# Kernel tuning notes

Hardware: AMD Instinct MI355X
Metric: run time of the kernel (lower is better)

The kernel has to match this reference:

```python
import jax, jax.numpy as jnp
from jax import lax
import numpy as np

T, B, N_POINTS = 512, 256, 34
N_HIDDEN, N_TARGET = 512, 16


def setup_inputs() -> dict:
    key = jax.random.key(0)
    ks = jax.random.split(key, 7)
    s_ih = 1.0 / np.sqrt(N_HIDDEN)
    return {
        "points": jax.random.normal(ks[0], (T, B, N_POINTS), dtype=jnp.float32),
        "W_ih": jax.random.uniform(ks[1], (4 * N_HIDDEN, N_POINTS), dtype=jnp.float32, minval=-s_ih, maxval=s_ih),
        "W_hh": jax.random.uniform(ks[2], (4 * N_HIDDEN, N_HIDDEN), dtype=jnp.float32, minval=-s_ih, maxval=s_ih),
        "b_ih": jax.random.uniform(ks[3], (4 * N_HIDDEN,), dtype=jnp.float32, minval=-s_ih, maxval=s_ih),
        "b_hh": jax.random.uniform(ks[4], (4 * N_HIDDEN,), dtype=jnp.float32, minval=-s_ih, maxval=s_ih),
        "W_lin": jax.random.uniform(ks[5], (N_TARGET, N_HIDDEN), dtype=jnp.float32, minval=-s_ih, maxval=s_ih),
        "b_lin": jax.random.uniform(ks[6], (N_TARGET,), dtype=jnp.float32, minval=-s_ih, maxval=s_ih),
    }


def reference(points, W_ih, W_hh, b_ih, b_hh, W_lin, b_lin):
    # points: [T, B, n_points]; PyTorch LSTM gate order: i, f, g, o
    H = W_hh.shape[1]
    Bsz = points.shape[1]
    # Precompute input projection for all timesteps: [T, B, 4H]
    x_proj = jnp.einsum('tbi,gi->tbg', points, W_ih) + b_ih + b_hh

    def step(carry, xt):
        h, c = carry
        gates = xt + h @ W_hh.T  # [B, 4H]
        i, f, g, o = jnp.split(gates, 4, axis=-1)
        i = jax.nn.sigmoid(i)
        f = jax.nn.sigmoid(f)
        g = jnp.tanh(g)
        o = jax.nn.sigmoid(o)
        c_new = f * c + i * g
        h_new = o * jnp.tanh(c_new)
        return (h_new, c_new), h_new

    h0 = jnp.zeros((Bsz, H), dtype=points.dtype)
    c0 = jnp.zeros((Bsz, H), dtype=points.dtype)
    _, hs = lax.scan(step, (h0, c0), x_proj)  # hs: [T, B, H]

    logits = hs.reshape(-1, H) @ W_lin.T + b_lin  # [T*B, n_target]
    return jax.nn.softmax(logits, axis=1)
```

## Files before the change

kernel.cpp:

```cpp
#include <hip/hip_runtime.h>

#define TT 512
#define BT 256
#define NP 34
#define HH 512
#define SENT 0xAAAAAAAAu

typedef short bf16x8 __attribute__((ext_vector_type(8)));
typedef float f32x4 __attribute__((ext_vector_type(4)));

static __device__ __forceinline__ unsigned short f2bf(float x) {
  unsigned int u = __float_as_uint(x);
  return (unsigned short)((u + 0x7fffu + ((u >> 16) & 1u)) >> 16);
}

template <int CTRL>
static __device__ __forceinline__ float dppq(float x) {
  return __int_as_float(
      __builtin_amdgcn_mov_dpp(__float_as_int(x), CTRL, 0xF, 0xF, true));
}

static __device__ __forceinline__ float rcpf(float x) {
  return __builtin_amdgcn_rcpf(x);
}

static __device__ __forceinline__ void load8_coh(const unsigned long long* p,
                                                 unsigned long long o[8]) {
  asm volatile(
      "global_load_dwordx2 %0, %8, off sc0 sc1\n\t"
      "global_load_dwordx2 %1, %9, off sc0 sc1\n\t"
      "global_load_dwordx2 %2, %10, off sc0 sc1\n\t"
      "global_load_dwordx2 %3, %11, off sc0 sc1\n\t"
      "global_load_dwordx2 %4, %12, off sc0 sc1\n\t"
      "global_load_dwordx2 %5, %13, off sc0 sc1\n\t"
      "global_load_dwordx2 %6, %14, off sc0 sc1\n\t"
      "global_load_dwordx2 %7, %15, off sc0 sc1\n\t"
      "s_waitcnt vmcnt(0)"
      : "=&v"(o[0]), "=&v"(o[1]), "=&v"(o[2]), "=&v"(o[3]),
        "=&v"(o[4]), "=&v"(o[5]), "=&v"(o[6]), "=&v"(o[7])
      : "v"(p), "v"(p + 256), "v"(p + 512), "v"(p + 768),
        "v"(p + 1024), "v"(p + 1280), "v"(p + 1536), "v"(p + 1792)
      : "memory");
}

__global__ void __launch_bounds__(256, 1) lstm_coop(
    const float* __restrict__ Whh, const float* __restrict__ Wih,
    const float* __restrict__ bih, const float* __restrict__ bhh,
    const unsigned short* __restrict__ Ax,
    unsigned short* hs)
{
  extern __shared__ char smem[];
  unsigned short* Wl = (unsigned short*)smem;
  unsigned short* stg = (unsigned short*)(smem + 131072);

  const int tid = threadIdx.x;
  const int g = blockIdx.x & 15;
  const int n = blockIdx.x >> 4;
  const int bbase = g * 16;

  for (int idx = tid; idx < 128 * 512; idx += 256) {
    int r = idx >> 9, k = idx & 511;
    int grow = (r & 3) * 512 + n * 32 + (r >> 2);
    float v = Whh[(size_t)grow * 512 + k];
    int c = k >> 3;
    Wl[r * 512 + ((c ^ (r & 7)) << 3) + (k & 7)] = f2bf(v);
  }

  const int lane = tid & 63;
  const int w = tid >> 6;
  const int m = lane & 15;
  const int ko = lane >> 4;
  const int r0 = 32 * w + m;
  const int q = m & 3;
  const int jj = m >> 2;
  const int j0 = 8 * w + jj;
  const int j1 = j0 + 4;
  const int mx = m & 7;

  float bi0[4], bi1[4];
#pragma unroll
  for (int gg = 0; gg < 4; ++gg) {
    int gr0 = gg * 512 + n * 32 + j0;
    int gr1 = gg * 512 + n * 32 + j1;
    bi0[gg] = bih[gr0] + bhh[gr0];
    bi1[gg] = bih[gr1] + bhh[gr1];
  }

  bf16x8 bx0a, bx1a, bx0b, bx1b;
  {
    int grow0 = q * 512 + n * 32 + j0;
    int grow1 = q * 512 + n * 32 + j1;
#pragma unroll
    for (int e = 0; e < 8; ++e) {
      int ka = 8 * ko + e;
      int kb = 32 + 8 * ko + e;
      bx0a[e] = (short)f2bf(Wih[grow0 * 34 + ka]);
      bx1a[e] = (short)f2bf(Wih[grow1 * 34 + ka]);
      bx0b[e] = (kb < NP) ? (short)f2bf(Wih[grow0 * 34 + kb]) : (short)0;
      bx1b[e] = (kb < NP) ? (short)f2bf(Wih[grow1 * 34 + kb]) : (short)0;
    }
  }
  __syncthreads();

  const bool q0 = (q == 0), q1 = (q == 1), q2 = (q == 2);
  float cc0 = 0.f, cc1 = 0.f;

  bf16x8 xv0, xv1;
  {
    const unsigned short* xb = Ax + ((size_t)0 * BT + bbase + m) * 64;
    xv0 = *(const bf16x8*)(xb + (ko << 3));
    xv1 = *(const bf16x8*)(xb + 32 + (ko << 3));
  }

  for (int t = 0; t < TT; ++t) {
    unsigned long long hv[8];
    if (t > 0) {
      const unsigned long long* pb =
          (const unsigned long long*)(hs + ((size_t)(t - 1) * BT + bbase) * HH) + tid;
      int guard = 0;
      for (;;) {
        load8_coh(pb, hv);
        unsigned ok = 1u;
#pragma unroll
        for (int u = 0; u < 8; ++u) {
          unsigned long long x = hv[u];
          ok &= ((unsigned)x != SENT) & ((unsigned)(x >> 32) != SENT) ? 1u : 0u;
        }
        if (ok) break;
        if (++guard > (1 << 18)) break;
      }
    } else {
#pragma unroll
      for (int u = 0; u < 8; ++u) hv[u] = 0ull;
    }

    bf16x8 xn0, xn1;
    {
      int tn = (t + 1 < TT) ? t + 1 : t;
      const unsigned short* xb = Ax + ((size_t)tn * BT + bbase + m) * 64;
      xn0 = *(const bf16x8*)(xb + (ko << 3));
      xn1 = *(const bf16x8*)(xb + 32 + (ko << 3));
    }

    unsigned short* st = stg + (t & 1) * 8192;
#pragma unroll
    for (int u = 0; u < 8; ++u) {
      int idx = u * 256 + tid;
      int mm = idx >> 7, cu = idx & 127;
      int c16 = cu >> 1, half = cu & 1;
      *(unsigned long long*)&st[mm * 512 + ((c16 ^ (mm & 7)) << 3) + (half << 2)] = hv[u];
    }
    __syncthreads();

    f32x4 a0a = {0.f, 0.f, 0.f, 0.f}, a0b = {0.f, 0.f, 0.f, 0.f};
    f32x4 a1a = {0.f, 0.f, 0.f, 0.f}, a1b = {0.f, 0.f, 0.f, 0.f};
#pragma unroll
    for (int s = 0; s < 16; ++s) {
      int cs = (((4 * s + ko) ^ mx) << 3);
      bf16x8 av = *(const bf16x8*)&st[m * 512 + cs];
      bf16x8 bv0 = *(const bf16x8*)&Wl[r0 * 512 + cs];
      bf16x8 bv1 = *(const bf16x8*)&Wl[(r0 + 16) * 512 + cs];
      if (s & 1) {
        a0b = __builtin_amdgcn_mfma_f32_16x16x32_bf16(av, bv0, a0b, 0, 0, 0);
        a1b = __builtin_amdgcn_mfma_f32_16x16x32_bf16(av, bv1, a1b, 0, 0, 0);
      } else {
        a0a = __builtin_amdgcn_mfma_f32_16x16x32_bf16(av, bv0, a0a, 0, 0, 0);
        a1a = __builtin_amdgcn_mfma_f32_16x16x32_bf16(av, bv1, a1a, 0, 0, 0);
      }
    }
    a0a = __builtin_amdgcn_mfma_f32_16x16x32_bf16(xv0, bx0a, a0a, 0, 0, 0);
    a1a = __builtin_amdgcn_mfma_f32_16x16x32_bf16(xv0, bx1a, a1a, 0, 0, 0);
    a0b = __builtin_amdgcn_mfma_f32_16x16x32_bf16(xv1, bx0b, a0b, 0, 0, 0);
    a1b = __builtin_amdgcn_mfma_f32_16x16x32_bf16(xv1, bx1b, a1b, 0, 0, 0);
    f32x4 A0 = a0a + a0b;
    f32x4 A1 = a1a + a1b;

    float own0 = q0 ? A0.x : q1 ? A0.y : q2 ? A0.z : A0.w;
    float t1s0 = q0 ? A0.w : q1 ? A0.x : q2 ? A0.y : A0.z;
    float t2s0 = q0 ? A0.z : q1 ? A0.w : q2 ? A0.x : A0.y;
    float t3s0 = q0 ? A0.y : q1 ? A0.z : q2 ? A0.w : A0.x;
    float r1_0 = dppq<0x39>(t1s0);
    float r2_0 = dppq<0x4E>(t2s0);
    float r3_0 = dppq<0x93>(t3s0);
    float own1 = q0 ? A1.x : q1 ? A1.y : q2 ? A1.z : A1.w;
    float t1s1 = q0 ? A1.w : q1 ? A1.x : q2 ? A1.y : A1.z;
    float t2s1 = q0 ? A1.z : q1 ? A1.w : q2 ? A1.x : A1.y;
    float t3s1 = q0 ? A1.y : q1 ? A1.z : q2 ? A1.w : A1.x;
    float r1_1 = dppq<0x39>(t1s1);
    float r2_1 = dppq<0x4E>(t2s1);
    float r3_1 = dppq<0x93>(t3s1);
    float gi0 = (q0 ? own0 : q1 ? r3_0 : q2 ? r2_0 : r1_0) + bi0[0];
    float gf0 = (q0 ? r1_0 : q1 ? own0 : q2 ? r3_0 : r2_0) + bi0[1];
    float gg0 = (q0 ? r2_0 : q1 ? r1_0 : q2 ? own0 : r3_0) + bi0[2];
    float go0 = (q0 ? r3_0 : q1 ? r2_0 : q2 ? r1_0 : own0) + bi0[3];
    float gi1 = (q0 ? own1 : q1 ? r3_1 : q2 ? r2_1 : r1_1) + bi1[0];
    float gf1 = (q0 ? r1_1 : q1 ? own1 : q2 ? r3_1 : r2_1) + bi1[1];
    float gg1 = (q0 ? r2_1 : q1 ? r1_1 : q2 ? own1 : r3_1) + bi1[2];
    float go1 = (q0 ? r3_1 : q1 ? r2_1 : q2 ? r1_1 : own1) + bi1[3];

    float ii0 = rcpf(1.f + __expf(-gi0));
    float ff0 = rcpf(1.f + __expf(-gf0));
    float tg0 = 2.f * rcpf(1.f + __expf(-2.f * gg0)) - 1.f;
    float oo0 = rcpf(1.f + __expf(-go0));
    cc0 = ff0 * cc0 + ii0 * tg0;
    float h0 = oo0 * (2.f * rcpf(1.f + __expf(-2.f * cc0)) - 1.f);

    float ii1 = rcpf(1.f + __expf(-gi1));
    float ff1 = rcpf(1.f + __expf(-gf1));
    float tg1 = 2.f * rcpf(1.f + __expf(-2.f * gg1)) - 1.f;
    float oo1 = rcpf(1.f + __expf(-go1));
    cc1 = ff1 * cc1 + ii1 * tg1;
    float h1 = oo1 * (2.f * rcpf(1.f + __expf(-2.f * cc1)) - 1.f);

    float h0p = __shfl_xor(h0, 4);
    float h1p = __shfl_xor(h1, 4);
    unsigned p0 = (unsigned)f2bf(h0) | ((unsigned)f2bf(h0p) << 16);
    unsigned p1 = (unsigned)f2bf(h1) | ((unsigned)f2bf(h1p) << 16);
    unsigned s0 = (unsigned)__shfl_xor((int)p0, 8);
    unsigned s1 = (unsigned)__shfl_xor((int)p1, 8);
    if (!(jj & 1)) {
      unsigned long long val = (jj == 0)
          ? (((unsigned long long)s0 << 32) | p0)
          : (((unsigned long long)p1 << 32) | s1);
      size_t uidx = ((size_t)t * BT + bbase + 4 * ko + q) * 128 +
                    8 * n + 2 * w + (jj >> 1);
      __hip_atomic_store((unsigned long long*)hs + uidx, val,
                         __ATOMIC_RELAXED, __HIP_MEMORY_SCOPE_AGENT);
    }
    xv0 = xn0;
    xv1 = xn1;
  }
}

__global__ void __launch_bounds__(256) prep_ax(const float* __restrict__ pts,
                                               unsigned short* __restrict__ Ax) {
  size_t i = (size_t)blockIdx.x * 256 + threadIdx.x;
  int k = (int)(i & 63);
  size_t tb = i >> 6;
  float v = (k < NP) ? pts[tb * NP + k] : 0.f;
  Ax[i] = f2bf(v);
}

__global__ void __launch_bounds__(256) head_kernel(const unsigned short* __restrict__ hs,
                                                   const float* __restrict__ Wlin,
                                                   const float* __restrict__ blin,
                                                   float* __restrict__ out) {
  __shared__ float wl[16 * 513];
  __shared__ float bl[16];
  __shared__ unsigned short hl[16 * 520];
  const int tid = threadIdx.x;
  for (int i = tid; i < 16 * 512; i += 256) wl[(i >> 9) * 513 + (i & 511)] = Wlin[i];
  if (tid < 16) bl[tid] = blin[tid];
  const size_t Rb = (size_t)blockIdx.x * 16;
  const uint4* gsrc = (const uint4*)(hs + Rb * 512);
#pragma unroll
  for (int j = 0; j < 4; ++j) {
    int e8 = tid + 256 * j;
    uint4 v = gsrc[e8];
    int r = e8 >> 6, k = (e8 & 63) << 3;
    *(uint4*)&hl[r * 520 + k] = v;
  }
  __syncthreads();
  const int r = tid >> 4, tg = tid & 15;
  float acc = bl[tg];
  const float* wp = &wl[tg * 513];
#pragma unroll 4
  for (int k8 = 0; k8 < 64; ++k8) {
    uint4 hv = *(const uint4*)&hl[r * 520 + (k8 << 3)];
    const float* w8 = wp + (k8 << 3);
    acc += __uint_as_float(hv.x << 16) * w8[0];
    acc += __uint_as_float(hv.x & 0xffff0000u) * w8[1];
    acc += __uint_as_float(hv.y << 16) * w8[2];
    acc += __uint_as_float(hv.y & 0xffff0000u) * w8[3];
    acc += __uint_as_float(hv.z << 16) * w8[4];
    acc += __uint_as_float(hv.z & 0xffff0000u) * w8[5];
    acc += __uint_as_float(hv.w << 16) * w8[6];
    acc += __uint_as_float(hv.w & 0xffff0000u) * w8[7];
  }
  float mx = acc;
#pragma unroll
  for (int d = 8; d; d >>= 1) mx = fmaxf(mx, __shfl_xor(mx, d, 16));
  float e = __expf(acc - mx);
  float sm = e;
#pragma unroll
  for (int d = 8; d; d >>= 1) sm += __shfl_xor(sm, d, 16);
  out[Rb * 16 + tid] = e / sm;
}

extern "C" void kernel_launch(void* const* d_in, const int* in_sizes, int n_in,
                              void* d_out, int out_size, void* d_ws, size_t ws_size,
                              hipStream_t stream) {
  (void)in_sizes; (void)n_in; (void)out_size; (void)ws_size;
  const float* pts  = (const float*)d_in[0];
  const float* Wih  = (const float*)d_in[1];
  const float* Whh  = (const float*)d_in[2];
  const float* bih  = (const float*)d_in[3];
  const float* bhh  = (const float*)d_in[4];
  const float* Wlin = (const float*)d_in[5];
  const float* blin = (const float*)d_in[6];
  float* out = (float*)d_out;
  char* ws = (char*)d_ws;
  unsigned short* hs = (unsigned short*)ws;
  unsigned short* Ax = (unsigned short*)(ws + 134217728);

  hipMemsetAsync(hs, 0xAA, 134217728, stream);
  prep_ax<<<32768, 256, 0, stream>>>(pts, Ax);
  (void)hipFuncSetAttribute((const void*)lstm_coop,
                            hipFuncAttributeMaxDynamicSharedMemorySize, 163840);
  void* args[6];
  args[0] = (void*)&Whh; args[1] = (void*)&Wih; args[2] = (void*)&bih;
  args[3] = (void*)&bhh; args[4] = (void*)&Ax;  args[5] = (void*)&hs;
  hipLaunchCooperativeKernel((void*)lstm_coop, dim3(256), dim3(256), args, 163840, stream);
  head_kernel<<<8192, 256, 0, stream>>>(hs, Wlin, blin, out);
}
```

Baseline: 1.461 ms.

## Split batch into two interleaved groups to overlap polling with compute

Repartitions the persistent LSTM so each block owns 16 hidden columns for two 16-row batch groups instead of 32 columns for one group. The recurrent h loads for one group are issued asynchronously while the other group's MFMA and gate math run, hiding the cross-block flag latency. In exchange each block holds half the recurrent weights in LDS and does two smaller sync/compute phases per step, adding barriers and producing smaller 8-byte stores.

```diff
diff --git a/kernel.cpp b/kernel.cpp
--- a/kernel.cpp
+++ b/kernel.cpp
@@ -22,6 +22,24 @@
 
 static __device__ __forceinline__ float rcpf(float x) {
   return __builtin_amdgcn_rcpf(x);
+}
+
+static __device__ __forceinline__ void issue8(const unsigned long long* p,
+                                              unsigned long long o[8]) {
+  asm volatile(
+      "global_load_dwordx2 %0, %8, off sc0 sc1\n\t"
+      "global_load_dwordx2 %1, %9, off sc0 sc1\n\t"
+      "global_load_dwordx2 %2, %10, off sc0 sc1\n\t"
+      "global_load_dwordx2 %3, %11, off sc0 sc1\n\t"
+      "global_load_dwordx2 %4, %12, off sc0 sc1\n\t"
+      "global_load_dwordx2 %5, %13, off sc0 sc1\n\t"
+      "global_load_dwordx2 %6, %14, off sc0 sc1\n\t"
+      "global_load_dwordx2 %7, %15, off sc0 sc1"
+      : "=&v"(o[0]), "=&v"(o[1]), "=&v"(o[2]), "=&v"(o[3]),
+        "=&v"(o[4]), "=&v"(o[5]), "=&v"(o[6]), "=&v"(o[7])
+      : "v"(p), "v"(p + 256), "v"(p + 512), "v"(p + 768),
+        "v"(p + 1024), "v"(p + 1280), "v"(p + 1536), "v"(p + 1792)
+      : "memory");
 }
 
 static __device__ __forceinline__ void load8_coh(const unsigned long long* p,
@@ -43,6 +61,17 @@
       : "memory");
 }
 
+static __device__ __forceinline__ unsigned validmask8(
+    const unsigned long long o[8]) {
+  unsigned ok = 1u;
+#pragma unroll
+  for (int u = 0; u < 8; ++u) {
+    unsigned long long x = o[u];
+    ok &= (((unsigned)x != SENT) & ((unsigned)(x >> 32) != SENT)) ? 1u : 0u;
+  }
+  return ok;
+}
+
 __global__ void __launch_bounds__(256, 1) lstm_coop(
     const float* __restrict__ Whh, const float* __restrict__ Wih,
     const float* __restrict__ bih, const float* __restrict__ bhh,
@@ -51,16 +80,18 @@
 {
   extern __shared__ char smem[];
   unsigned short* Wl = (unsigned short*)smem;
-  unsigned short* stg = (unsigned short*)(smem + 131072);
+  unsigned short* stgA = (unsigned short*)(smem + 65536);
+  unsigned short* stgB = (unsigned short*)(smem + 98304);
 
   const int tid = threadIdx.x;
-  const int g = blockIdx.x & 15;
-  const int n = blockIdx.x >> 4;
-  const int bbase = g * 16;
-
-  for (int idx = tid; idx < 128 * 512; idx += 256) {
+  const int n2 = blockIdx.x & 31;
+  const int p = blockIdx.x >> 5;
+  const int bbA = p * 32;
+  const int bbB = p * 32 + 16;
+
+  for (int idx = tid; idx < 64 * 512; idx += 256) {
     int r = idx >> 9, k = idx & 511;
-    int grow = (r & 3) * 512 + n * 32 + (r >> 2);
+    int grow = (r & 3) * 512 + n2 * 16 + (r >> 2);
     float v = Whh[(size_t)grow * 512 + k];
     int c = k >> 3;
     Wl[r * 512 + ((c ^ (r & 7)) << 3) + (k & 7)] = f2bf(v);
@@ -70,79 +101,63 @@
   const int w = tid >> 6;
   const int m = lane & 15;
   const int ko = lane >> 4;
-  const int r0 = 32 * w + m;
+  const int r0 = 16 * w + m;
   const int q = m & 3;
   const int jj = m >> 2;
-  const int j0 = 8 * w + jj;
-  const int j1 = j0 + 4;
+  const int col = n2 * 16 + 4 * w + jj;
   const int mx = m & 7;
-
-  float bi0[4], bi1[4];
+  const bool q0 = (q == 0), q1 = (q == 1), q2 = (q == 2);
+
+  float bi[4];
 #pragma unroll
   for (int gg = 0; gg < 4; ++gg) {
-    int gr0 = gg * 512 + n * 32 + j0;
-    int gr1 = gg * 512 + n * 32 + j1;
-    bi0[gg] = bih[gr0] + bhh[gr0];
-    bi1[gg] = bih[gr1] + bhh[gr1];
-  }
-
-  bf16x8 bx0a, bx1a, bx0b, bx1b;
+    int gr = gg * 512 + col;
+    bi[gg] = bih[gr] + bhh[gr];
+  }
+
+  bf16x8 bxa, bxb;
   {
-    int grow0 = q * 512 + n * 32 + j0;
-    int grow1 = q * 512 + n * 32 + j1;
+    int grow = (r0 & 3) * 512 + n2 * 16 + (r0 >> 2);
 #pragma unroll
     for (int e = 0; e < 8; ++e) {
       int ka = 8 * ko + e;
       int kb = 32 + 8 * ko + e;
-      bx0a[e] = (short)f2bf(Wih[grow0 * 34 + ka]);
-      bx1a[e] = (short)f2bf(Wih[grow1 * 34 + ka]);
-      bx0b[e] = (kb < NP) ? (short)f2bf(Wih[grow0 * 34 + kb]) : (short)0;
-      bx1b[e] = (kb < NP) ? (short)f2bf(Wih[grow1 * 34 + kb]) : (short)0;
+      bxa[e] = (short)f2bf(Wih[grow * 34 + ka]);
+      bxb[e] = (kb < NP) ? (short)f2bf(Wih[grow * 34 + kb]) : (short)0;
     }
   }
   __syncthreads();
 
-  const bool q0 = (q == 0), q1 = (q == 1), q2 = (q == 2);
-  float cc0 = 0.f, cc1 = 0.f;
-
-  bf16x8 xv0, xv1;
+  float ccA = 0.f, ccB = 0.f;
+  unsigned long long pollA[8], pollB[8];
+
+  bf16x8 xvA0, xvA1, xvB0, xvB1;
   {
-    const unsigned short* xb = Ax + ((size_t)0 * BT + bbase + m) * 64;
-    xv0 = *(const bf16x8*)(xb + (ko << 3));
-    xv1 = *(const bf16x8*)(xb + 32 + (ko << 3));
+    const unsigned short* xb = Ax + ((size_t)0 * BT + bbA + m) * 64;
+    xvA0 = *(const bf16x8*)(xb + (ko << 3));
+    xvA1 = *(const bf16x8*)(xb + 32 + (ko << 3));
   }
 
   for (int t = 0; t < TT; ++t) {
-    unsigned long long hv[8];
+    unsigned long long* hv = pollA;
     if (t > 0) {
       const unsigned long long* pb =
-          (const unsigned long long*)(hs + ((size_t)(t - 1) * BT + bbase) * HH) + tid;
-      int guard = 0;
-      for (;;) {
-        load8_coh(pb, hv);
-        unsigned ok = 1u;
-#pragma unroll
-        for (int u = 0; u < 8; ++u) {
-          unsigned long long x = hv[u];
-          ok &= ((unsigned)x != SENT) & ((unsigned)(x >> 32) != SENT) ? 1u : 0u;
+          (const unsigned long long*)(hs + ((size_t)(t - 1) * BT + bbA) * HH) + tid;
+      asm volatile("s_waitcnt vmcnt(0)" ::: "memory");
+      __builtin_amdgcn_sched_barrier(0);
+      if (!validmask8(pollA)) {
+        int guard = 0;
+        for (;;) {
+          load8_coh(pb, pollA);
+          if (validmask8(pollA)) break;
+          if (++guard > (1 << 18)) break;
         }
-        if (ok) break;
-        if (++guard > (1 << 18)) break;
       }
     } else {
 #pragma unroll
-      for (int u = 0; u < 8; ++u) hv[u] = 0ull;
-    }
-
-    bf16x8 xn0, xn1;
-    {
-      int tn = (t + 1 < TT) ? t + 1 : t;
-      const unsigned short* xb = Ax + ((size_t)tn * BT + bbase + m) * 64;
-      xn0 = *(const bf16x8*)(xb + (ko << 3));
-      xn1 = *(const bf16x8*)(xb + 32 + (ko << 3));
-    }
-
-    unsigned short* st = stg + (t & 1) * 8192;
+      for (int u = 0; u < 8; ++u) pollA[u] = 0ull;
+    }
+    unsigned short* st = stgA + (t & 1) * 8192;
 #pragma unroll
     for (int u = 0; u < 8; ++u) {
       int idx = u * 256 + tid;
@@ -151,84 +166,135 @@
       *(unsigned long long*)&st[mm * 512 + ((c16 ^ (mm & 7)) << 3) + (half << 2)] = hv[u];
     }
     __syncthreads();
-
-    f32x4 a0a = {0.f, 0.f, 0.f, 0.f}, a0b = {0.f, 0.f, 0.f, 0.f};
-    f32x4 a1a = {0.f, 0.f, 0.f, 0.f}, a1b = {0.f, 0.f, 0.f, 0.f};
-#pragma unroll
-    for (int s = 0; s < 16; ++s) {
-      int cs = (((4 * s + ko) ^ mx) << 3);
-      bf16x8 av = *(const bf16x8*)&st[m * 512 + cs];
-      bf16x8 bv0 = *(const bf16x8*)&Wl[r0 * 512 + cs];
-      bf16x8 bv1 = *(const bf16x8*)&Wl[(r0 + 16) * 512 + cs];
-      if (s & 1) {
-        a0b = __builtin_amdgcn_mfma_f32_16x16x32_bf16(av, bv0, a0b, 0, 0, 0);
-        a1b = __builtin_amdgcn_mfma_f32_16x16x32_bf16(av, bv1, a1b, 0, 0, 0);
-      } else {
-        a0a = __builtin_amdgcn_mfma_f32_16x16x32_bf16(av, bv0, a0a, 0, 0, 0);
-        a1a = __builtin_amdgcn_mfma_f32_16x16x32_bf16(av, bv1, a1a, 0, 0, 0);
-      }
-    }
-    a0a = __builtin_amdgcn_mfma_f32_16x16x32_bf16(xv0, bx0a, a0a, 0, 0, 0);
-    a1a = __builtin_amdgcn_mfma_f32_16x16x32_bf16(xv0, bx1a, a1a, 0, 0, 0);
-    a0b = __builtin_amdgcn_mfma_f32_16x16x32_bf16(xv1, bx0b, a0b, 0, 0, 0);
-    a1b = __builtin_amdgcn_mfma_f32_16x16x32_bf16(xv1, bx1b, a1b, 0, 0, 0);
-    f32x4 A0 = a0a + a0b;
-    f32x4 A1 = a1a + a1b;
-
-    float own0 = q0 ? A0.x : q1 ? A0.y : q2 ? A0.z : A0.w;
-    float t1s0 = q0 ? A0.w : q1 ? A0.x : q2 ? A0.y : A0.z;
-    float t2s0 = q0 ? A0.z : q1 ? A0.w : q2 ? A0.x : A0.y;
-    float t3s0 = q0 ? A0.y : q1 ? A0.z : q2 ? A0.w : A0.x;
-    float r1_0 = dppq<0x39>(t1s0);
-    float r2_0 = dppq<0x4E>(t2s0);
-    float r3_0 = dppq<0x93>(t3s0);
-    float own1 = q0 ? A1.x : q1 ? A1.y : q2 ? A1.z : A1.w;
-    float t1s1 = q0 ? A1.w : q1 ? A1.x : q2 ? A1.y : A1.z;
-    float t2s1 = q0 ? A1.z : q1 ? A1.w : q2 ? A1.x : A1.y;
-    float t3s1 = q0 ? A1.y : q1 ? A1.z : q2 ? A1.w : A1.x;
-    float r1_1 = dppq<0x39>(t1s1);
-    float r2_1 = dppq<0x4E>(t2s1);
-    float r3_1 = dppq<0x93>(t3s1);
-    float gi0 = (q0 ? own0 : q1 ? r3_0 : q2 ? r2_0 : r1_0) + bi0[0];
-    float gf0 = (q0 ? r1_0 : q1 ? own0 : q2 ? r3_0 : r2_0) + bi0[1];
-    float gg0 = (q0 ? r2_0 : q1 ? r1_0 : q2 ? own0 : r3_0) + bi0[2];
-    float go0 = (q0 ? r3_0 : q1 ? r2_0 : q2 ? r1_0 : own0) + bi0[3];
-    float gi1 = (q0 ? own1 : q1 ? r3_1 : q2 ? r2_1 : r1_1) + bi1[0];
-    float gf1 = (q0 ? r1_1 : q1 ? own1 : q2 ? r3_1 : r2_1) + bi1[1];
-    float gg1 = (q0 ? r2_1 : q1 ? r1_1 : q2 ? own1 : r3_1) + bi1[2];
-    float go1 = (q0 ? r3_1 : q1 ? r2_1 : q2 ? r1_1 : own1) + bi1[3];
-
-    float ii0 = rcpf(1.f + __expf(-gi0));
-    float ff0 = rcpf(1.f + __expf(-gf0));
-    float tg0 = 2.f * rcpf(1.f + __expf(-2.f * gg0)) - 1.f;
-    float oo0 = rcpf(1.f + __expf(-go0));
-    cc0 = ff0 * cc0 + ii0 * tg0;
-    float h0 = oo0 * (2.f * rcpf(1.f + __expf(-2.f * cc0)) - 1.f);
-
-    float ii1 = rcpf(1.f + __expf(-gi1));
-    float ff1 = rcpf(1.f + __expf(-gf1));
-    float tg1 = 2.f * rcpf(1.f + __expf(-2.f * gg1)) - 1.f;
-    float oo1 = rcpf(1.f + __expf(-go1));
-    cc1 = ff1 * cc1 + ii1 * tg1;
-    float h1 = oo1 * (2.f * rcpf(1.f + __expf(-2.f * cc1)) - 1.f);
-
-    float h0p = __shfl_xor(h0, 4);
-    float h1p = __shfl_xor(h1, 4);
-    unsigned p0 = (unsigned)f2bf(h0) | ((unsigned)f2bf(h0p) << 16);
-    unsigned p1 = (unsigned)f2bf(h1) | ((unsigned)f2bf(h1p) << 16);
-    unsigned s0 = (unsigned)__shfl_xor((int)p0, 8);
-    unsigned s1 = (unsigned)__shfl_xor((int)p1, 8);
-    if (!(jj & 1)) {
-      unsigned long long val = (jj == 0)
-          ? (((unsigned long long)s0 << 32) | p0)
-          : (((unsigned long long)p1 << 32) | s1);
-      size_t uidx = ((size_t)t * BT + bbase + 4 * ko + q) * 128 +
-                    8 * n + 2 * w + (jj >> 1);
-      __hip_atomic_store((unsigned long long*)hs + uidx, val,
-                         __ATOMIC_RELAXED, __HIP_MEMORY_SCOPE_AGENT);
-    }
-    xv0 = xn0;
-    xv1 = xn1;
+    if (t > 0) {
+      const unsigned long long* pb =
+          (const unsigned long long*)(hs + ((size_t)(t - 1) * BT + bbB) * HH) + tid;
+      issue8(pb, pollB);
+    }
+    {
+      const unsigned short* xb = Ax + ((size_t)t * BT + bbB + m) * 64;
+      xvB0 = *(const bf16x8*)(xb + (ko << 3));
+      xvB1 = *(const bf16x8*)(xb + 32 + (ko << 3));
+    }
+    {
+      f32x4 aa = {0.f, 0.f, 0.f, 0.f}, ab = {0.f, 0.f, 0.f, 0.f};
+#pragma unroll
+      for (int s = 0; s < 16; ++s) {
+        int cs = (((4 * s + ko) ^ mx) << 3);
+        bf16x8 av = *(const bf16x8*)&st[m * 512 + cs];
+        bf16x8 bv = *(const bf16x8*)&Wl[r0 * 512 + cs];
+        if (s & 1) ab = __builtin_amdgcn_mfma_f32_16x16x32_bf16(av, bv, ab, 0, 0, 0);
+        else       aa = __builtin_amdgcn_mfma_f32_16x16x32_bf16(av, bv, aa, 0, 0, 0);
+      }
+      aa = __builtin_amdgcn_mfma_f32_16x16x32_bf16(xvA0, bxa, aa, 0, 0, 0);
+      ab = __builtin_amdgcn_mfma_f32_16x16x32_bf16(xvA1, bxb, ab, 0, 0, 0);
+      f32x4 A = aa + ab;
+      float own = q0 ? A.x : q1 ? A.y : q2 ? A.z : A.w;
+      float t1s = q0 ? A.w : q1 ? A.x : q2 ? A.y : A.z;
+      float t2s = q0 ? A.z : q1 ? A.w : q2 ? A.x : A.y;
+      float t3s = q0 ? A.y : q1 ? A.z : q2 ? A.w : A.x;
+      float r1 = dppq<0x39>(t1s);
+      float r2 = dppq<0x4E>(t2s);
+      float r3 = dppq<0x93>(t3s);
+      float gi = (q0 ? own : q1 ? r3 : q2 ? r2 : r1) + bi[0];
+      float gf = (q0 ? r1 : q1 ? own : q2 ? r3 : r2) + bi[1];
+      float gg = (q0 ? r2 : q1 ? r1 : q2 ? own : r3) + bi[2];
+      float go = (q0 ? r3 : q1 ? r2 : q2 ? r1 : own) + bi[3];
+      float ii = rcpf(1.f + __expf(-gi));
+      float ff = rcpf(1.f + __expf(-gf));
+      float tg = 2.f * rcpf(1.f + __expf(-2.f * gg)) - 1.f;
+      float oo = rcpf(1.f + __expf(-go));
+      ccA = ff * ccA + ii * tg;
+      float h = oo * (2.f * rcpf(1.f + __expf(-2.f * ccA)) - 1.f);
+      float hp = __shfl_xor(h, 4);
+      unsigned pr = (unsigned)f2bf(h) | ((unsigned)f2bf(hp) << 16);
+      unsigned sr = (unsigned)__shfl_xor((int)pr, 8);
+      if (jj == 0) {
+        unsigned long long val = (((unsigned long long)sr << 32) | pr);
+        size_t uidx = ((size_t)t * BT + bbA + 4 * ko + q) * 128 + 4 * n2 + w;
+        __hip_atomic_store((unsigned long long*)hs + uidx, val,
+                           __ATOMIC_RELAXED, __HIP_MEMORY_SCOPE_AGENT);
+      }
+    }
+
+    hv = pollB;
+    if (t > 0) {
+      const unsigned long long* pb =
+          (const unsigned long long*)(hs + ((size_t)(t - 1) * BT + bbB) * HH) + tid;
+      asm volatile("s_waitcnt vmcnt(0)" ::: "memory");
+      __builtin_amdgcn_sched_barrier(0);
+      if (!validmask8(pollB)) {
+        int guard = 0;
+        for (;;) {
+          load8_coh(pb, pollB);
+          if (validmask8(pollB)) break;
+          if (++guard > (1 << 18)) break;
+        }
+      }
+    } else {
+#pragma unroll
+      for (int u = 0; u < 8; ++u) pollB[u] = 0ull;
+    }
+    st = stgB + (t & 1) * 8192;
+#pragma unroll
+    for (int u = 0; u < 8; ++u) {
+      int idx = u * 256 + tid;
+      int mm = idx >> 7, cu = idx & 127;
+      int c16 = cu >> 1, half = cu & 1;
+      *(unsigned long long*)&st[mm * 512 + ((c16 ^ (mm & 7)) << 3) + (half << 2)] = hv[u];
+    }
+    __syncthreads();
+    {
+      const unsigned long long* pb =
+          (const unsigned long long*)(hs + ((size_t)t * BT + bbA) * HH) + tid;
+      issue8(pb, pollA);
+    }
+    {
+      int tn = (t + 1 < TT) ? t + 1 : t;
+      const unsigned short* xb = Ax + ((size_t)tn * BT + bbA + m) * 64;
+      xvA0 = *(const bf16x8*)(xb + (ko << 3));
+      xvA1 = *(const bf16x8*)(xb + 32 + (ko << 3));
+    }
+    {
+      f32x4 aa = {0.f, 0.f, 0.f, 0.f}, ab = {0.f, 0.f, 0.f, 0.f};
+#pragma unroll
+      for (int s = 0; s < 16; ++s) {
+        int cs = (((4 * s + ko) ^ mx) << 3);
+        bf16x8 av = *(const bf16x8*)&st[m * 512 + cs];
+        bf16x8 bv = *(const bf16x8*)&Wl[r0 * 512 + cs];
+        if (s & 1) ab = __builtin_amdgcn_mfma_f32_16x16x32_bf16(av, bv, ab, 0, 0, 0);
+        else       aa = __builtin_amdgcn_mfma_f32_16x16x32_bf16(av, bv, aa, 0, 0, 0);
+      }
+      aa = __builtin_amdgcn_mfma_f32_16x16x32_bf16(xvB0, bxa, aa, 0, 0, 0);
+      ab = __builtin_amdgcn_mfma_f32_16x16x32_bf16(xvB1, bxb, ab, 0, 0, 0);
+      f32x4 A = aa + ab;
+      float own = q0 ? A.x : q1 ? A.y : q2 ? A.z : A.w;
+      float t1s = q0 ? A.w : q1 ? A.x : q2 ? A.y : A.z;
+      float t2s = q0 ? A.z : q1 ? A.w : q2 ? A.x : A.y;
+      float t3s = q0 ? A.y : q1 ? A.z : q2 ? A.w : A.x;
+      float r1 = dppq<0x39>(t1s);
+      float r2 = dppq<0x4E>(t2s);
+      float r3 = dppq<0x93>(t3s);
+      float gi = (q0 ? own : q1 ? r3 : q2 ? r2 : r1) + bi[0];
+      float gf = (q0 ? r1 : q1 ? own : q2 ? r3 : r2) + bi[1];
+      float gg = (q0 ? r2 : q1 ? r1 : q2 ? own : r3) + bi[2];
+      float go = (q0 ? r3 : q1 ? r2 : q2 ? r1 : own) + bi[3];
+      float ii = rcpf(1.f + __expf(-gi));
+      float ff = rcpf(1.f + __expf(-gf));
+      float tg = 2.f * rcpf(1.f + __expf(-2.f * gg)) - 1.f;
+      float oo = rcpf(1.f + __expf(-go));
+      ccB = ff * ccB + ii * tg;
+      float h = oo * (2.f * rcpf(1.f + __expf(-2.f * ccB)) - 1.f);
+      float hp = __shfl_xor(h, 4);
+      unsigned pr = (unsigned)f2bf(h) | ((unsigned)f2bf(hp) << 16);
+      unsigned sr = (unsigned)__shfl_xor((int)pr, 8);
+      if (jj == 0) {
+        unsigned long long val = (((unsigned long long)sr << 32) | pr);
+        size_t uidx = ((size_t)t * BT + bbB + 4 * ko + q) * 128 + 4 * n2 + w;
+        __hip_atomic_store((unsigned long long*)hs + uidx, val,
+                           __ATOMIC_RELAXED, __HIP_MEMORY_SCOPE_AGENT);
+      }
+    }
   }
 }
 
@@ -306,10 +372,10 @@
   hipMemsetAsync(hs, 0xAA, 134217728, stream);
   prep_ax<<<32768, 256, 0, stream>>>(pts, Ax);
   (void)hipFuncSetAttribute((const void*)lstm_coop,
-                            hipFuncAttributeMaxDynamicSharedMemorySize, 163840);
+                            hipFuncAttributeMaxDynamicSharedMemorySize, 131072);
   void* args[6];
   args[0] = (void*)&Whh; args[1] = (void*)&Wih; args[2] = (void*)&bih;
   args[3] = (void*)&bhh; args[4] = (void*)&Ax;  args[5] = (void*)&hs;
-  hipLaunchCooperativeKernel((void*)lstm_coop, dim3(256), dim3(256), args, 163840, stream);
+  hipLaunchCooperativeKernel((void*)lstm_coop, dim3(256), dim3(256), args, 131072, stream);
   head_kernel<<<8192, 256, 0, stream>>>(hs, Wlin, blin, out);
 }
```

New measurement: 2.237 ms. 53.1% more time.
